# Kernel tuning notes

Hardware: AMD Instinct MI355X
Metric: run time of the kernel (lower is better)

The kernel has to match this reference:

```python
import jax, jax.numpy as jnp
import numpy as np
from jax import lax

H_HID, W_HID = 8, 12
N_PAIR = H_HID * W_HID   # 96
NF = 32                  # mlp_nfilters
C_FEAT = 512 + 2         # phi_im channels + (x,y) coords


def _conv_relu(x, w, b):
    # 3x3 conv, stride 1, SAME padding (SingleConvBlock), then ReLU
    y = lax.conv_general_dilated(x, w, (1, 1), 'SAME',
                                 dimension_numbers=('NCHW', 'OIHW', 'NCHW'))
    return jax.nn.relu(y + b[None, :, None, None])


def _maxpool2(x):
    return lax.reduce_window(x, -jnp.inf, lax.max, (1, 1, 2, 2), (1, 1, 2, 2), 'VALID')


def setup_inputs() -> dict:
    key = jax.random.key(0)
    ks = jax.random.split(key, 16)
    d = {}
    d['x'] = jax.random.normal(ks[0], (4, 3, 64, 96), jnp.float32)
    d['sen_embed'] = jax.random.normal(ks[1], (4, 384), jnp.float32)

    def p(k, shape, fan_in):
        return (jax.random.normal(k, shape, jnp.float32) / np.float32(np.sqrt(fan_in)))

    d['enc1_w'] = p(ks[2], (64, 3, 3, 3), 3 * 9);      d['enc1_b'] = p(ks[3], (64,), 64)
    d['enc2_w'] = p(ks[4], (128, 64, 3, 3), 64 * 9);   d['enc2_b'] = p(ks[5], (128,), 128)
    d['enc3_w'] = p(ks[6], (256, 128, 3, 3), 128 * 9); d['enc3_b'] = p(ks[7], (256,), 256)
    d['enc4_w'] = p(ks[8], (512, 256, 3, 3), 256 * 9); d['enc4_b'] = p(ks[9], (512,), 512)
    d['g1_w'] = p(ks[10], (1412, 256), 1412);          d['g1_b'] = p(ks[11], (256,), 256)
    d['g2_w'] = p(ks[12], (256, 256), 256);            d['g2_b'] = p(ks[13], (256,), 256)
    d['g3_w'] = p(ks[14], (256, N_PAIR * NF), 256);    d['g3_b'] = p(ks[15], (N_PAIR * NF,), N_PAIR * NF)
    return d


def _forward(x, sen_embed, enc1_w, enc1_b, enc2_w, enc2_b, enc3_w, enc3_b,
             enc4_w, enc4_b, g1_w, g1_b, g2_w, g2_b, g3_w, g3_b):
    # ---- conv encoder ----
    e1 = _conv_relu(x, enc1_w, enc1_b)                     # [B,64,64,96]
    e2 = _conv_relu(_maxpool2(e1), enc2_w, enc2_b)         # [B,128,32,48]
    e3 = _conv_relu(_maxpool2(e2), enc3_w, enc3_b)         # [B,256,16,24]
    phi_im = _conv_relu(_maxpool2(e3), enc4_w, enc4_b)     # [B,512,8,12]
    B = phi_im.shape[0]

    # ---- coordinate grid (matches torch.meshgrid default 'ij' then reshape) ----
    xc = jnp.linspace(-1.0, 1.0, W_HID, dtype=phi_im.dtype)
    yc = jnp.linspace(-1.0, 1.0, H_HID, dtype=phi_im.dtype)
    xg, yg = jnp.meshgrid(xc, yc, indexing='ij')           # each [12,8]
    coord = jnp.stack([xg.reshape(H_HID, W_HID), yg.reshape(H_HID, W_HID)], axis=0)
    coord = jnp.broadcast_to(coord[None], (B, 2, H_HID, W_HID))

    # per-location features F: [B, n_pair, 514]
    F = jnp.concatenate([phi_im, coord], axis=1).reshape(B, C_FEAT, N_PAIR).transpose(0, 2, 1)

    # ---- all-pairs relation network ----
    # pair feature at (a,c) = concat(F[c], F[a], sen_embed); exploit linearity of first
    # Linear to avoid materializing the [B,n,n,1412] concat tensor (same math).
    A, Bm, Cm = g1_w[:C_FEAT], g1_w[C_FEAT:2 * C_FEAT], g1_w[2 * C_FEAT:]
    u = F @ A                                # i-part,  [B,n,256]
    v = F @ Bm                               # j-part,  [B,n,256]
    ws = sen_embed @ Cm + g1_b               # sentence part, [B,256]
    h1 = jax.nn.relu(u[:, None, :, :] + v[:, :, None, :] + ws[:, None, None, :])  # [B,n,n,256]
    h2 = jax.nn.relu(h1 @ g2_w + g2_b)                                           # [B,n,n,256]
    out = jax.nn.relu(h2 @ g3_w + g3_b)                                          # [B,n,n,3072]

    # sum over all n_pair^2 pairs, reshape to feature map [B,32,8,12]
    phi = out.sum(axis=(1, 2)).reshape(B, NF, H_HID, W_HID)
    return phi


def reference(x, sen_embed, enc1_w, enc1_b, enc2_w, enc2_b, enc3_w, enc3_b,
              enc4_w, enc4_b, g1_w, g1_b, g2_w, g2_b, g3_w, g3_b):
    return _forward(x, sen_embed, enc1_w, enc1_b, enc2_w, enc2_b, enc3_w, enc3_b,
                    enc4_w, enc4_b, g1_w, g1_b, g2_w, g2_b, g3_w, g3_b)
```

## Files before the change

kernel.cpp:

```cpp
#include <hip/hip_runtime.h>
#include <hip/hip_bf16.h>

using bf16 = __hip_bfloat16;
typedef __attribute__((ext_vector_type(8))) short short8;
typedef __attribute__((ext_vector_type(4))) float f32x4;

static __device__ __forceinline__ bf16 f2b(float x) { return __float2bfloat16(x); }
static __device__ __forceinline__ float b2f(bf16 x) { return __bfloat162float(x); }
static __device__ __forceinline__ short fb(float x) {
  bf16 h = __float2bfloat16(fmaxf(x, 0.f));
  return *(short*)&h;
}

static __device__ __forceinline__ void gload_lds16(const void* g, void* l) {
  auto gp = (const __attribute__((address_space(1))) unsigned int*)g;
  auto lp = (__attribute__((address_space(3))) unsigned int*)l;
  __builtin_amdgcn_global_load_lds(gp, lp, 16, 0, 0);
}

__global__ void prep_all_kernel(const float* __restrict__ x, const float* __restrict__ w1,
                                const float* __restrict__ b1, bf16* __restrict__ p1,
                                const float* __restrict__ w2, const float* __restrict__ w3,
                                const float* __restrict__ w4, const float* __restrict__ g1w,
                                const float* __restrict__ sen, float* __restrict__ outz,
                                bf16* __restrict__ w2r, bf16* __restrict__ w3r,
                                bf16* __restrict__ w4r, bf16* __restrict__ wuv,
                                bf16* __restrict__ Fe, float* __restrict__ zb,
                                const float* __restrict__ g2w, const float* __restrict__ g3w,
                                bf16* __restrict__ w2t, bf16* __restrict__ w3t) {
  __shared__ float wl[27 * 64];
  __shared__ bf16 tt[32][33];
  int bid = blockIdx.x;
  int tid = threadIdx.x;
  if (bid < 1536) {
    const int H = 64, W = 96, HW = H * W;
    for (int idx = tid; idx < 27 * 64; idx += 256) {
      int k = idx >> 6, oc_ = idx & 63;
      wl[idx] = w1[oc_ * 27 + k];
    }
    __syncthreads();
    int oc = tid & 63;
    int pp = bid * 4 + (tid >> 6);
    int b = pp / 1536, rem = pp - b * 1536;
    int yp = rem / 48, xp = rem - yp * 48;
    int y0 = 2 * yp - 1, x0 = 2 * xp - 1;
    float win[3][4][4];
    #pragma unroll
    for (int ic = 0; ic < 3; ++ic) {
      const float* xsrc = x + ((size_t)b * 3 + ic) * HW;
      #pragma unroll
      for (int dy = 0; dy < 4; ++dy) {
        int yy = y0 + dy;
        #pragma unroll
        for (int dx = 0; dx < 4; ++dx) {
          int xx = x0 + dx;
          win[ic][dy][dx] = (yy >= 0 && yy < H && xx >= 0 && xx < W) ? xsrc[yy * W + xx] : 0.f;
        }
      }
    }
    float cmax = -1e30f;
    #pragma unroll
    for (int sy = 0; sy < 2; ++sy)
      #pragma unroll
      for (int sx = 0; sx < 2; ++sx) {
        float acc = 0.f;
        #pragma unroll
        for (int ic = 0; ic < 3; ++ic)
          #pragma unroll
          for (int ky = 0; ky < 3; ++ky)
            #pragma unroll
            for (int kx = 0; kx < 3; ++kx)
              acc += win[ic][sy + ky][sx + kx] * wl[(ic * 9 + ky * 3 + kx) * 64 + oc];
        cmax = fmaxf(cmax, acc);
      }
    p1[(size_t)pp * 64 + oc] = f2b(fmaxf(cmax + b1[oc], 0.f));
  } else if (bid < 9601) {
    const int S1 = 73728, S2 = S1 + 294912, S3 = S2 + 1179648, S4 = S3 + 442368,
              S5 = S4 + 12288, S6 = S5 + 24576, S7 = S6 + 36864, S8 = S7 + 64;
    int i = (bid - 1536) * 256 + tid;
    if (i < S1) {
      int j = i, K = 576, IC = 64;
      int oc = j / K, r = j - oc * K, tap = r / IC, ic = r - tap * IC;
      w2r[j] = f2b(w2[((size_t)oc * IC + ic) * 9 + tap]);
    } else if (i < S2) {
      int j = i - S1, K = 1152, IC = 128;
      int oc = j / K, r = j - oc * K, tap = r / IC, ic = r - tap * IC;
      w3r[j] = f2b(w3[((size_t)oc * IC + ic) * 9 + tap]);
    } else if (i < S3) {
      int j = i - S2, K = 2304, IC = 256;
      int oc = j / K, r = j - oc * K, tap = r / IC, ic = r - tap * IC;
      w4r[j] = f2b(w4[((size_t)oc * IC + ic) * 9 + tap]);
    } else if (i < S4) {
      int j = i - S3;
      int n = j / 576, c = j - n * 576;
      float val = 0.f;
      if (n < 256)      { if (c < 514) val = g1w[(size_t)c * 256 + n]; }
      else if (n < 512) { if (c < 514) val = g1w[(size_t)(514 + c) * 256 + (n - 256)]; }
      else              { if (c < 384) val = g1w[(size_t)(1028 + c) * 256 + (n - 512)]; }
      wuv[j] = f2b(val);
    } else if (i < S5) {
      outz[i - S4] = 0.f;
    } else if (i < S6) {
      int j = i - S5;
      int r = j >> 6, cc = j & 63;
      int p = r % 96;
      float val = 0.f;
      if (cc == 0) val = -1.0f + 2.0f * (float)(p / 8) / 11.0f;
      else if (cc == 1) val = -1.0f + 2.0f * (float)(p % 8) / 7.0f;
      Fe[(size_t)r * 576 + 512 + cc] = f2b(val);
    } else if (i < S7) {
      int j = i - S6;
      int r = j / 576, c = j - r * 576;
      float val = (r < 4 && c < 384) ? sen[r * 384 + c] : 0.f;
      Fe[(size_t)(384 + r) * 576 + c] = f2b(val);
    } else if (i < S8) {
      zb[i - S7] = 0.f;
    }
  } else {
    int b2 = bid - 9601;
    const float* in;
    bf16* out;
    int R = 256, C, c0, r0;
    if (b2 < 64) { in = g2w; out = w2t; C = 256; c0 = (b2 & 7) * 32; r0 = (b2 >> 3) * 32; }
    else { b2 -= 64; in = g3w; out = w3t; C = 3072; c0 = (b2 % 96) * 32; r0 = (b2 / 96) * 32; }
    int xq = tid & 31, yq = tid >> 5;
    for (int yy = yq; yy < 32; yy += 8) {
      int r = r0 + yy, c = c0 + xq;
      if (r < R && c < C) tt[yy][xq] = f2b(in[(size_t)r * C + c]);
    }
    __syncthreads();
    for (int yy = yq; yy < 32; yy += 8) {
      int c = c0 + yy, r = r0 + xq;
      if (r < R && c < C) out[(size_t)c * R + r] = tt[xq][yy];
    }
  }
}

template <int CBITS, bool POOL>
__launch_bounds__(256)
__global__ void gemm_conv_kernel(const bf16* __restrict__ pin, const bf16* __restrict__ Wt,
                                 const float* __restrict__ bias, bf16* __restrict__ outb,
                                 const bf16* __restrict__ zbuf,
                                 int Hi, int Wi, int N, int ldout) {
  const int C = 1 << CBITS;
  const int K = 9 << CBITS;
  int m0 = blockIdx.y * 64, n0 = blockIdx.x * 64;
  __shared__ __align__(16) short A_lds[2][64 * 64];
  __shared__ __align__(16) short B_lds[2][64 * 64];
  int tid = threadIdx.x, w = tid >> 6, l = tid & 63;
  int quad = l >> 4, l16 = l & 15;
  f32x4 acc[4];
  #pragma unroll
  for (int nt = 0; nt < 4; ++nt)
    #pragma unroll
    for (int e = 0; e < 4; ++e) acc[nt][e] = 0.f;

  int lrow = l >> 3;
  int c_sw = (l & 7) ^ lrow;
  int ybase[2], xbase[2], bidx[2];
  #pragma unroll
  for (int i = 0; i < 2; ++i) {
    int row = m0 + w * 16 + i * 8 + lrow;
    if (POOL) {
      int pg = row >> 2, sub = row & 3;
      int Wh = Wi >> 1, HW2 = (Hi >> 1) * Wh;
      int b = pg / HW2, rem = pg - b * HW2;
      int py = rem / Wh, px = rem - py * Wh;
      bidx[i] = b; ybase[i] = 2 * py + (sub >> 1); xbase[i] = 2 * px + (sub & 1);
    } else {
      int HW = Hi * Wi;
      int b = row / HW, pix = row - b * HW;
      int yy = pix / Wi;
      bidx[i] = b; ybase[i] = yy; xbase[i] = pix - yy * Wi;
    }
  }
  const bf16* bg = Wt + (size_t)(n0 + w * 16 + lrow) * K + c_sw * 8;

  auto stage = [&](int kc, int buf) {
    int colt = kc + c_sw * 8;
    int tap = colt >> CBITS, cc = colt & (C - 1);
    int ty = tap / 3, tx = tap - 3 * ty;
    short* al = &A_lds[buf][((size_t)w * 128 + l) * 8];
    short* bl = &B_lds[buf][((size_t)w * 128 + l) * 8];
    #pragma unroll
    for (int i = 0; i < 2; ++i) {
      int yy = ybase[i] + ty - 1, xx = xbase[i] + tx - 1;
      const bf16* asrc = (yy >= 0 && yy < Hi && xx >= 0 && xx < Wi)
          ? pin + ((((size_t)(bidx[i] * Hi + yy)) * Wi + xx) << CBITS) + cc
          : zbuf;
      gload_lds16(asrc, al + i * 512);
      gload_lds16(bg + kc + (size_t)i * 8 * K, bl + i * 512);
    }
  };

  stage(0, 0);
  const int NK = K >> 6;
  for (int ik = 0; ik < NK; ++ik) {
    int buf = ik & 1;
    __syncthreads();
    if (ik + 1 < NK) stage((ik + 1) * 64, buf ^ 1);
    #pragma unroll
    for (int ks = 0; ks < 64; ks += 32) {
      int cb = (ks >> 3) + quad;
      int mr = w * 16 + l16;
      short8 af = *(const short8*)&A_lds[buf][mr * 64 + ((cb ^ (mr & 7)) * 8)];
      #pragma unroll
      for (int nt = 0; nt < 4; ++nt) {
        int nr = nt * 16 + l16;
        short8 bf2 = *(const short8*)&B_lds[buf][nr * 64 + ((cb ^ (nr & 7)) * 8)];
        acc[nt] = __builtin_amdgcn_mfma_f32_16x16x32_bf16(af, bf2, acc[nt], 0, 0, 0);
      }
    }
  }
  if (POOL) {
    int pg = (m0 + w * 16 + quad * 4) >> 2;
    #pragma unroll
    for (int nt = 0; nt < 4; ++nt) {
      int gcol = n0 + nt * 16 + l16;
      float bv = bias[gcol];
      float m = fmaxf(fmaxf(acc[nt][0], acc[nt][1]), fmaxf(acc[nt][2], acc[nt][3]));
      outb[(size_t)pg * N + gcol] = f2b(fmaxf(m + bv, 0.f));
    }
  } else {
    #pragma unroll
    for (int nt = 0; nt < 4; ++nt) {
      int gcol = n0 + nt * 16 + l16;
      float bv = bias[gcol];
      #pragma unroll
      for (int r = 0; r < 4; ++r) {
        int grow = m0 + w * 16 + quad * 4 + r;
        outb[(size_t)grow * ldout + gcol] = f2b(fmaxf(acc[nt][r] + bv, 0.f));
      }
    }
  }
}

__launch_bounds__(256)
__global__ void gemm64_kernel(const bf16* __restrict__ A, const bf16* __restrict__ Wt,
                              float* __restrict__ outf, int K, int ldout) {
  int m0 = blockIdx.y * 64, n0 = blockIdx.x * 64;
  __shared__ __align__(16) short A_lds[2][64 * 64];
  __shared__ __align__(16) short B_lds[2][64 * 64];
  int tid = threadIdx.x, w = tid >> 6, l = tid & 63;
  int quad = l >> 4, l16 = l & 15;
  f32x4 acc[4];
  #pragma unroll
  for (int nt = 0; nt < 4; ++nt)
    #pragma unroll
    for (int e = 0; e < 4; ++e) acc[nt][e] = 0.f;

  int lrow = l >> 3;
  int c_sw = (l & 7) ^ lrow;
  const bf16* ag = A + (size_t)(m0 + w * 16 + lrow) * K + c_sw * 8;
  const bf16* bg = Wt + (size_t)(n0 + w * 16 + lrow) * K + c_sw * 8;

  auto stage = [&](int kc, int buf) {
    short* al = &A_lds[buf][((size_t)w * 128 + l) * 8];
    short* bl = &B_lds[buf][((size_t)w * 128 + l) * 8];
    #pragma unroll
    for (int i = 0; i < 2; ++i) {
      gload_lds16(ag + kc + (size_t)i * 8 * K, al + i * 512);
      gload_lds16(bg + kc + (size_t)i * 8 * K, bl + i * 512);
    }
  };

  stage(0, 0);
  const int NK = K >> 6;
  for (int ik = 0; ik < NK; ++ik) {
    int buf = ik & 1;
    __syncthreads();
    if (ik + 1 < NK) stage((ik + 1) * 64, buf ^ 1);
    #pragma unroll
    for (int ks = 0; ks < 64; ks += 32) {
      int cb = (ks >> 3) + quad;
      int mr = w * 16 + l16;
      short8 af = *(const short8*)&A_lds[buf][mr * 64 + ((cb ^ (mr & 7)) * 8)];
      #pragma unroll
      for (int nt = 0; nt < 4; ++nt) {
        int nr = nt * 16 + l16;
        short8 bf2 = *(const short8*)&B_lds[buf][nr * 64 + ((cb ^ (nr & 7)) * 8)];
        acc[nt] = __builtin_amdgcn_mfma_f32_16x16x32_bf16(af, bf2, acc[nt], 0, 0, 0);
      }
    }
  }
  #pragma unroll
  for (int nt = 0; nt < 4; ++nt) {
    int gcol = n0 + nt * 16 + l16;
    #pragma unroll
    for (int r = 0; r < 4; ++r) {
      int grow = m0 + w * 16 + quad * 4 + r;
      outf[(size_t)grow * ldout + gcol] = acc[nt][r];
    }
  }
}

__launch_bounds__(256)
__global__ void gemm2_kernel(const float* __restrict__ uvws, const float* __restrict__ g1b,
                             const bf16* __restrict__ w2t, const float* __restrict__ g2b,
                             bf16* __restrict__ h2) {
  int b = blockIdx.z;
  int m0 = blockIdx.y * 128;
  int n0 = blockIdx.x * 128;
  __shared__ __align__(16) short A_lds[128 * 64];
  __shared__ __align__(16) short B_lds[128 * 64];
  __shared__ __align__(16) float wsl[256];
  int tid = threadIdx.x, w = tid >> 6, l = tid & 63;
  int quad = l >> 4, l16 = l & 15;
  int mw = (w >> 1) * 64, nw = (w & 1) * 64;
  f32x4 acc[4][4];
  #pragma unroll
  for (int i = 0; i < 4; ++i)
    #pragma unroll
    for (int j = 0; j < 4; ++j)
      #pragma unroll
      for (int e = 0; e < 4; ++e) acc[i][j][e] = 0.f;

  wsl[tid] = uvws[(size_t)(384 + b) * 768 + 512 + tid] + g1b[tid];

  int lrow = l >> 3;
  int c_sw = (l & 7) ^ lrow;
  const bf16* bg = w2t + (size_t)(n0 + w * 32 + lrow) * 256 + c_sw * 8;
  short* bl = B_lds + ((size_t)w * 256 + l) * 8;

  int row = tid >> 1, ks0 = (tid & 1) * 32;
  int m = m0 + row;
  int i_idx = m / 96, j_idx = m - i_idx * 96;
  const float* up = uvws + (size_t)(b * 96 + j_idx) * 768 + ks0;
  const float* vp = uvws + (size_t)(b * 96 + i_idx) * 768 + 256 + ks0;
  __syncthreads();

  for (int kc = 0; kc < 256; kc += 64) {
    if (kc) __syncthreads();
    #pragma unroll
    for (int i = 0; i < 4; ++i)
      gload_lds16(bg + kc + (size_t)i * 8 * 256, bl + i * 512);
    {
      const float4* u4 = (const float4*)(up + kc);
      const float4* v4 = (const float4*)(vp + kc);
      const float4* w4 = (const float4*)&wsl[kc + ks0];
      #pragma unroll
      for (int ch = 0; ch < 4; ++ch) {
        short8 pack;
        #pragma unroll
        for (int q = 0; q < 2; ++q) {
          float4 uu = u4[ch * 2 + q], vv = v4[ch * 2 + q], ww = w4[ch * 2 + q];
          pack[q * 4 + 0] = fb(uu.x + vv.x + ww.x);
          pack[q * 4 + 1] = fb(uu.y + vv.y + ww.y);
          pack[q * 4 + 2] = fb(uu.z + vv.z + ww.z);
          pack[q * 4 + 3] = fb(uu.w + vv.w + ww.w);
        }
        int lc = (ks0 >> 3) + ch;
        *(short8*)&A_lds[row * 64 + ((lc ^ (row & 7)) * 8)] = pack;
      }
    }
    __syncthreads();
    #pragma unroll
    for (int ks = 0; ks < 64; ks += 32) {
      int cb = (ks >> 3) + quad;
      short8 af[4], bfr[4];
      #pragma unroll
      for (int mt = 0; mt < 4; ++mt) {
        int mr = mw + mt * 16 + l16;
        af[mt] = *(const short8*)&A_lds[mr * 64 + ((cb ^ (mr & 7)) * 8)];
      }
      #pragma unroll
      for (int nt = 0; nt < 4; ++nt) {
        int nr = nw + nt * 16 + l16;
        bfr[nt] = *(const short8*)&B_lds[nr * 64 + ((cb ^ (nr & 7)) * 8)];
      }
      #pragma unroll
      for (int mt = 0; mt < 4; ++mt)
        #pragma unroll
        for (int nt = 0; nt < 4; ++nt)
          acc[mt][nt] = __builtin_amdgcn_mfma_f32_16x16x32_bf16(af[mt], bfr[nt], acc[mt][nt], 0, 0, 0);
    }
  }
  bf16* h2b = h2 + (size_t)b * 9216 * 256;
  #pragma unroll
  for (int nt = 0; nt < 4; ++nt) {
    int gcol = n0 + nw + nt * 16 + l16;
    float bias = g2b[gcol];
    #pragma unroll
    for (int mt = 0; mt < 4; ++mt) {
      #pragma unroll
      for (int r = 0; r < 4; ++r) {
        int grow = m0 + mw + mt * 16 + quad * 4 + r;
        h2b[(size_t)grow * 256 + gcol] = f2b(fmaxf(acc[mt][nt][r] + bias, 0.f));
      }
    }
  }
}

__launch_bounds__(256)
__global__ void gemm3_kernel(const bf16* __restrict__ h2, const bf16* __restrict__ w3t,
                             const float* __restrict__ g3b, float* __restrict__ phi) {
  int g = blockIdx.x;
  int x = g & 7, s = g >> 3;
  int grp = s / 24;
  int nIdx = s - grp * 24;
  int mb = grp * 8 + x;
  int b = mb / 72;
  int m0 = (mb - b * 72) * 128;
  int n0 = nIdx * 128;
  __shared__ __align__(16) short A_lds[128 * 64];
  __shared__ __align__(16) short B_lds[128 * 64];
  int tid = threadIdx.x, w = tid >> 6, l = tid & 63;
  int quad = l >> 4, l16 = l & 15;
  int mw = (w >> 1) * 64, nw = (w & 1) * 64;
  f32x4 acc[4][4];
  #pragma unroll
  for (int i = 0; i < 4; ++i)
    #pragma unroll
    for (int j = 0; j < 4; ++j)
      #pragma unroll
      for (int e = 0; e < 4; ++e) acc[i][j][e] = 0.f;

  const int K = 256;
  int lrow = l >> 3;
  int c_sw = (l & 7) ^ lrow;
  const bf16* ag = h2 + (size_t)(b * 9216 + m0 + w * 32 + lrow) * K + c_sw * 8;
  const bf16* bg = w3t + (size_t)(n0 + w * 32 + lrow) * K + c_sw * 8;
  short* al = A_lds + ((size_t)w * 256 + l) * 8;
  short* bl = B_lds + ((size_t)w * 256 + l) * 8;

  for (int kc = 0; kc < K; kc += 64) {
    if (kc) __syncthreads();
    #pragma unroll
    for (int i = 0; i < 4; ++i) {
      gload_lds16(ag + kc + (size_t)i * 8 * K, al + i * 512);
      gload_lds16(bg + kc + (size_t)i * 8 * K, bl + i * 512);
    }
    __syncthreads();
    #pragma unroll
    for (int ks = 0; ks < 64; ks += 32) {
      int cb = (ks >> 3) + quad;
      short8 af[4], bfr[4];
      #pragma unroll
      for (int mt = 0; mt < 4; ++mt) {
        int mr = mw + mt * 16 + l16;
        af[mt] = *(const short8*)&A_lds[mr * 64 + ((cb ^ (mr & 7)) * 8)];
      }
      #pragma unroll
      for (int nt = 0; nt < 4; ++nt) {
        int nr = nw + nt * 16 + l16;
        bfr[nt] = *(const short8*)&B_lds[nr * 64 + ((cb ^ (nr & 7)) * 8)];
      }
      #pragma unroll
      for (int mt = 0; mt < 4; ++mt)
        #pragma unroll
        for (int nt = 0; nt < 4; ++nt)
          acc[mt][nt] = __builtin_amdgcn_mfma_f32_16x16x32_bf16(af[mt], bfr[nt], acc[mt][nt], 0, 0, 0);
    }
  }
  #pragma unroll
  for (int nt = 0; nt < 4; ++nt) {
    int gcol = n0 + nw + nt * 16 + l16;
    float bias = g3b[gcol];
    float s2 = 0.f;
    #pragma unroll
    for (int mt = 0; mt < 4; ++mt)
      #pragma unroll
      for (int r = 0; r < 4; ++r)
        s2 += fmaxf(acc[mt][nt][r] + bias, 0.f);
    s2 += __shfl_xor(s2, 16, 64);
    s2 += __shfl_xor(s2, 32, 64);
    if (quad == 0) atomicAdd(&phi[b * 3072 + gcol], s2);
  }
}

extern "C" void kernel_launch(void* const* d_in, const int* in_sizes, int n_in,
                              void* d_out, int out_size, void* d_ws, size_t ws_size,
                              hipStream_t stream) {
  const float* x   = (const float*)d_in[0];
  const float* sen = (const float*)d_in[1];
  const float* w1  = (const float*)d_in[2];
  const float* b1  = (const float*)d_in[3];
  const float* w2  = (const float*)d_in[4];
  const float* b2  = (const float*)d_in[5];
  const float* w3  = (const float*)d_in[6];
  const float* b3  = (const float*)d_in[7];
  const float* w4  = (const float*)d_in[8];
  const float* b4  = (const float*)d_in[9];
  const float* g1w = (const float*)d_in[10];
  const float* g1b = (const float*)d_in[11];
  const float* g2w = (const float*)d_in[12];
  const float* g2b = (const float*)d_in[13];
  const float* g3w = (const float*)d_in[14];
  const float* g3b = (const float*)d_in[15];
  float* out = (float*)d_out;

  char* wsp = (char*)d_ws;
  size_t off = 0;
  auto alloc = [&](size_t bytes) {
    char* p = wsp + off;
    off += (bytes + 255) & ~(size_t)255;
    return (void*)p;
  };
  bf16* p1   = (bf16*)alloc((size_t)6144 * 64 * 2);
  bf16* p2   = (bf16*)alloc((size_t)1536 * 128 * 2);
  bf16* p3   = (bf16*)alloc((size_t)384 * 256 * 2);
  bf16* Fe   = (bf16*)alloc((size_t)448 * 576 * 2);
  bf16* wuv  = (bf16*)alloc((size_t)768 * 576 * 2);
  float* uvws = (float*)alloc((size_t)448 * 768 * 4);
  bf16* w2r  = (bf16*)alloc((size_t)128 * 576 * 2);
  bf16* w3r  = (bf16*)alloc((size_t)256 * 1152 * 2);
  bf16* w4r  = (bf16*)alloc((size_t)512 * 2304 * 2);
  bf16* w2t  = (bf16*)alloc((size_t)256 * 256 * 2);
  bf16* w3t  = (bf16*)alloc((size_t)3072 * 256 * 2);
  bf16* h2   = (bf16*)alloc((size_t)4 * 9216 * 256 * 2);
  float* zbuf = (float*)alloc((size_t)256);

  prep_all_kernel<<<dim3(10433), 256, 0, stream>>>(x, w1, b1, p1, w2, w3, w4, g1w, sen, out,
                                                   w2r, w3r, w4r, wuv, Fe, zbuf, g2w, g3w, w2t, w3t);

  gemm_conv_kernel<6, true><<<dim3(2, 96), 256, 0, stream>>>(p1, w2r, b2, p2, (const bf16*)zbuf, 32, 48, 128, 128);
  gemm_conv_kernel<7, true><<<dim3(4, 24), 256, 0, stream>>>(p2, w3r, b3, p3, (const bf16*)zbuf, 16, 24, 256, 256);
  gemm_conv_kernel<8, false><<<dim3(8, 6), 256, 0, stream>>>(p3, w4r, b4, Fe, (const bf16*)zbuf, 8, 12, 512, 576);

  gemm64_kernel<<<dim3(12, 7), 256, 0, stream>>>(Fe, wuv, uvws, 576, 768);
  gemm2_kernel<<<dim3(2, 72, 4), 256, 0, stream>>>(uvws, g1b, w2t, g2b, h2);
  gemm3_kernel<<<dim3(6912), 256, 0, stream>>>(h2, w3t, g3b, out);
}
```

Baseline: 240.7 us.

## Fuse all stages into one persistent cooperative kernel with grid syncs

Replaces the seven separate kernel launches (prep, three conv GEMMs, uv GEMM, pair GEMM2, GEMM3) with a single cooperative persistent kernel. Blocks loop over per-stage task indices and use grid.sync between stages, sharing one LDS allocation. This removes inter-launch gaps and launch overhead. The cost is grid-wide barriers, a single combined register/LDS footprint that may lower occupancy for the heavier stages, and fixed persistent grid sizing (up to 3 blocks per CU).

```diff
diff --git a/kernel.cpp b/kernel.cpp
--- a/kernel.cpp
+++ b/kernel.cpp
@@ -1,12 +1,13 @@
 #include <hip/hip_runtime.h>
 #include <hip/hip_bf16.h>
-
+#include <hip/hip_cooperative_groups.h>
+
+namespace cg = cooperative_groups;
 using bf16 = __hip_bfloat16;
 typedef __attribute__((ext_vector_type(8))) short short8;
 typedef __attribute__((ext_vector_type(4))) float f32x4;
 
 static __device__ __forceinline__ bf16 f2b(float x) { return __float2bfloat16(x); }
-static __device__ __forceinline__ float b2f(bf16 x) { return __bfloat162float(x); }
 static __device__ __forceinline__ short fb(float x) {
   bf16 h = __float2bfloat16(fmaxf(x, 0.f));
   return *(short*)&h;
@@ -18,36 +19,33 @@
   __builtin_amdgcn_global_load_lds(gp, lp, 16, 0, 0);
 }
 
-__global__ void prep_all_kernel(const float* __restrict__ x, const float* __restrict__ w1,
-                                const float* __restrict__ b1, bf16* __restrict__ p1,
-                                const float* __restrict__ w2, const float* __restrict__ w3,
-                                const float* __restrict__ w4, const float* __restrict__ g1w,
-                                const float* __restrict__ sen, float* __restrict__ outz,
-                                bf16* __restrict__ w2r, bf16* __restrict__ w3r,
-                                bf16* __restrict__ w4r, bf16* __restrict__ wuv,
-                                bf16* __restrict__ Fe, float* __restrict__ zb,
-                                const float* __restrict__ g2w, const float* __restrict__ g3w,
-                                bf16* __restrict__ w2t, bf16* __restrict__ w3t) {
-  __shared__ float wl[27 * 64];
-  __shared__ bf16 tt[32][33];
-  int bid = blockIdx.x;
-  int tid = threadIdx.x;
-  if (bid < 1536) {
+struct MegaParams {
+  const float *x, *sen, *w1, *b1, *w2, *b2, *w3, *b3, *w4, *b4;
+  const float *g1w, *g1b, *g2w, *g2b, *g3w, *g3b;
+  float* out;
+  bf16 *p1, *p2, *p3, *Fe, *wuv, *w2r, *w3r, *w4r, *w2t, *w3t, *h2;
+  float *uvws, *zbuf;
+};
+
+static __device__ void prep_task(const MegaParams& P, int t, int tid, short* LA, short* LB) {
+  if (t < 1536) {
+    float* wl = (float*)LA;
+    __syncthreads();
     const int H = 64, W = 96, HW = H * W;
     for (int idx = tid; idx < 27 * 64; idx += 256) {
       int k = idx >> 6, oc_ = idx & 63;
-      wl[idx] = w1[oc_ * 27 + k];
+      wl[idx] = P.w1[oc_ * 27 + k];
     }
     __syncthreads();
     int oc = tid & 63;
-    int pp = bid * 4 + (tid >> 6);
+    int pp = t * 4 + (tid >> 6);
     int b = pp / 1536, rem = pp - b * 1536;
     int yp = rem / 48, xp = rem - yp * 48;
     int y0 = 2 * yp - 1, x0 = 2 * xp - 1;
     float win[3][4][4];
     #pragma unroll
     for (int ic = 0; ic < 3; ++ic) {
-      const float* xsrc = x + ((size_t)b * 3 + ic) * HW;
+      const float* xsrc = P.x + ((size_t)b * 3 + ic) * HW;
       #pragma unroll
       for (int dy = 0; dy < 4; ++dy) {
         int yy = y0 + dy;
@@ -73,33 +71,33 @@
               acc += win[ic][sy + ky][sx + kx] * wl[(ic * 9 + ky * 3 + kx) * 64 + oc];
         cmax = fmaxf(cmax, acc);
       }
-    p1[(size_t)pp * 64 + oc] = f2b(fmaxf(cmax + b1[oc], 0.f));
-  } else if (bid < 9601) {
+    P.p1[(size_t)pp * 64 + oc] = f2b(fmaxf(cmax + P.b1[oc], 0.f));
+  } else if (t < 9601) {
     const int S1 = 73728, S2 = S1 + 294912, S3 = S2 + 1179648, S4 = S3 + 442368,
               S5 = S4 + 12288, S6 = S5 + 24576, S7 = S6 + 36864, S8 = S7 + 64;
-    int i = (bid - 1536) * 256 + tid;
+    int i = (t - 1536) * 256 + tid;
     if (i < S1) {
       int j = i, K = 576, IC = 64;
       int oc = j / K, r = j - oc * K, tap = r / IC, ic = r - tap * IC;
-      w2r[j] = f2b(w2[((size_t)oc * IC + ic) * 9 + tap]);
+      P.w2r[j] = f2b(P.w2[((size_t)oc * IC + ic) * 9 + tap]);
     } else if (i < S2) {
       int j = i - S1, K = 1152, IC = 128;
       int oc = j / K, r = j - oc * K, tap = r / IC, ic = r - tap * IC;
-      w3r[j] = f2b(w3[((size_t)oc * IC + ic) * 9 + tap]);
+      P.w3r[j] = f2b(P.w3[((size_t)oc * IC + ic) * 9 + tap]);
     } else if (i < S3) {
       int j = i - S2, K = 2304, IC = 256;
       int oc = j / K, r = j - oc * K, tap = r / IC, ic = r - tap * IC;
-      w4r[j] = f2b(w4[((size_t)oc * IC + ic) * 9 + tap]);
+      P.w4r[j] = f2b(P.w4[((size_t)oc * IC + ic) * 9 + tap]);
     } else if (i < S4) {
       int j = i - S3;
       int n = j / 576, c = j - n * 576;
       float val = 0.f;
-      if (n < 256)      { if (c < 514) val = g1w[(size_t)c * 256 + n]; }
-      else if (n < 512) { if (c < 514) val = g1w[(size_t)(514 + c) * 256 + (n - 256)]; }
-      else              { if (c < 384) val = g1w[(size_t)(1028 + c) * 256 + (n - 512)]; }
-      wuv[j] = f2b(val);
+      if (n < 256)      { if (c < 514) val = P.g1w[(size_t)c * 256 + n]; }
+      else if (n < 512) { if (c < 514) val = P.g1w[(size_t)(514 + c) * 256 + (n - 256)]; }
+      else              { if (c < 384) val = P.g1w[(size_t)(1028 + c) * 256 + (n - 512)]; }
+      P.wuv[j] = f2b(val);
     } else if (i < S5) {
-      outz[i - S4] = 0.f;
+      P.out[i - S4] = 0.f;
     } else if (i < S6) {
       int j = i - S5;
       int r = j >> 6, cc = j & 63;
@@ -107,22 +105,24 @@
       float val = 0.f;
       if (cc == 0) val = -1.0f + 2.0f * (float)(p / 8) / 11.0f;
       else if (cc == 1) val = -1.0f + 2.0f * (float)(p % 8) / 7.0f;
-      Fe[(size_t)r * 576 + 512 + cc] = f2b(val);
+      P.Fe[(size_t)r * 576 + 512 + cc] = f2b(val);
     } else if (i < S7) {
       int j = i - S6;
       int r = j / 576, c = j - r * 576;
-      float val = (r < 4 && c < 384) ? sen[r * 384 + c] : 0.f;
-      Fe[(size_t)(384 + r) * 576 + c] = f2b(val);
+      float val = (r < 4 && c < 384) ? P.sen[r * 384 + c] : 0.f;
+      P.Fe[(size_t)(384 + r) * 576 + c] = f2b(val);
     } else if (i < S8) {
-      zb[i - S7] = 0.f;
+      P.zbuf[i - S7] = 0.f;
     }
   } else {
-    int b2 = bid - 9601;
+    bf16 (*tt)[33] = (bf16(*)[33])LB;
+    __syncthreads();
+    int b2 = t - 9601;
     const float* in;
     bf16* out;
     int R = 256, C, c0, r0;
-    if (b2 < 64) { in = g2w; out = w2t; C = 256; c0 = (b2 & 7) * 32; r0 = (b2 >> 3) * 32; }
-    else { b2 -= 64; in = g3w; out = w3t; C = 3072; c0 = (b2 % 96) * 32; r0 = (b2 / 96) * 32; }
+    if (b2 < 64) { in = P.g2w; out = P.w2t; C = 256; c0 = (b2 & 7) * 32; r0 = (b2 >> 3) * 32; }
+    else { b2 -= 64; in = P.g3w; out = P.w3t; C = 3072; c0 = (b2 % 96) * 32; r0 = (b2 / 96) * 32; }
     int xq = tid & 31, yq = tid >> 5;
     for (int yy = yq; yy < 32; yy += 8) {
       int r = r0 + yy, c = c0 + xq;
@@ -137,17 +137,13 @@
 }
 
 template <int CBITS, bool POOL>
-__launch_bounds__(256)
-__global__ void gemm_conv_kernel(const bf16* __restrict__ pin, const bf16* __restrict__ Wt,
-                                 const float* __restrict__ bias, bf16* __restrict__ outb,
-                                 const bf16* __restrict__ zbuf,
-                                 int Hi, int Wi, int N, int ldout) {
+static __device__ void conv_task(const bf16* pin, const bf16* Wt, const float* bias,
+                                 bf16* outb, const bf16* zbuf, int Hi, int Wi, int N, int ldout,
+                                 int nIdx, int mIdx, int tid, short* LA, short* LB) {
   const int C = 1 << CBITS;
   const int K = 9 << CBITS;
-  int m0 = blockIdx.y * 64, n0 = blockIdx.x * 64;
-  __shared__ __align__(16) short A_lds[2][64 * 64];
-  __shared__ __align__(16) short B_lds[2][64 * 64];
-  int tid = threadIdx.x, w = tid >> 6, l = tid & 63;
+  int m0 = mIdx * 64, n0 = nIdx * 64;
+  int w = tid >> 6, l = tid & 63;
   int quad = l >> 4, l16 = l & 15;
   f32x4 acc[4];
   #pragma unroll
@@ -180,8 +176,8 @@
     int colt = kc + c_sw * 8;
     int tap = colt >> CBITS, cc = colt & (C - 1);
     int ty = tap / 3, tx = tap - 3 * ty;
-    short* al = &A_lds[buf][((size_t)w * 128 + l) * 8];
-    short* bl = &B_lds[buf][((size_t)w * 128 + l) * 8];
+    short* al = LA + buf * 4096 + ((size_t)w * 128 + l) * 8;
+    short* bl = LB + buf * 4096 + ((size_t)w * 128 + l) * 8;
     #pragma unroll
     for (int i = 0; i < 2; ++i) {
       int yy = ybase[i] + ty - 1, xx = xbase[i] + tx - 1;
@@ -193,6 +189,7 @@
     }
   };
 
+  __syncthreads();
   stage(0, 0);
   const int NK = K >> 6;
   for (int ik = 0; ik < NK; ++ik) {
@@ -203,11 +200,11 @@
     for (int ks = 0; ks < 64; ks += 32) {
       int cb = (ks >> 3) + quad;
       int mr = w * 16 + l16;
-      short8 af = *(const short8*)&A_lds[buf][mr * 64 + ((cb ^ (mr & 7)) * 8)];
+      short8 af = *(const short8*)&LA[buf * 4096 + mr * 64 + ((cb ^ (mr & 7)) * 8)];
       #pragma unroll
       for (int nt = 0; nt < 4; ++nt) {
         int nr = nt * 16 + l16;
-        short8 bf2 = *(const short8*)&B_lds[buf][nr * 64 + ((cb ^ (nr & 7)) * 8)];
+        short8 bf2 = *(const short8*)&LB[buf * 4096 + nr * 64 + ((cb ^ (nr & 7)) * 8)];
         acc[nt] = __builtin_amdgcn_mfma_f32_16x16x32_bf16(af, bf2, acc[nt], 0, 0, 0);
       }
     }
@@ -235,13 +232,10 @@
   }
 }
 
-__launch_bounds__(256)
-__global__ void gemm64_kernel(const bf16* __restrict__ A, const bf16* __restrict__ Wt,
-                              float* __restrict__ outf, int K, int ldout) {
-  int m0 = blockIdx.y * 64, n0 = blockIdx.x * 64;
-  __shared__ __align__(16) short A_lds[2][64 * 64];
-  __shared__ __align__(16) short B_lds[2][64 * 64];
-  int tid = threadIdx.x, w = tid >> 6, l = tid & 63;
+static __device__ void gemm64_task(const bf16* A, const bf16* Wt, float* outf, int K, int ldout,
+                                   int nIdx, int mIdx, int tid, short* LA, short* LB) {
+  int m0 = mIdx * 64, n0 = nIdx * 64;
+  int w = tid >> 6, l = tid & 63;
   int quad = l >> 4, l16 = l & 15;
   f32x4 acc[4];
   #pragma unroll
@@ -255,8 +249,8 @@
   const bf16* bg = Wt + (size_t)(n0 + w * 16 + lrow) * K + c_sw * 8;
 
   auto stage = [&](int kc, int buf) {
-    short* al = &A_lds[buf][((size_t)w * 128 + l) * 8];
-    short* bl = &B_lds[buf][((size_t)w * 128 + l) * 8];
+    short* al = LA + buf * 4096 + ((size_t)w * 128 + l) * 8;
+    short* bl = LB + buf * 4096 + ((size_t)w * 128 + l) * 8;
     #pragma unroll
     for (int i = 0; i < 2; ++i) {
       gload_lds16(ag + kc + (size_t)i * 8 * K, al + i * 512);
@@ -264,6 +258,7 @@
     }
   };
 
+  __syncthreads();
   stage(0, 0);
   const int NK = K >> 6;
   for (int ik = 0; ik < NK; ++ik) {
@@ -274,11 +269,11 @@
     for (int ks = 0; ks < 64; ks += 32) {
       int cb = (ks >> 3) + quad;
       int mr = w * 16 + l16;
-      short8 af = *(const short8*)&A_lds[buf][mr * 64 + ((cb ^ (mr & 7)) * 8)];
+      short8 af = *(const short8*)&LA[buf * 4096 + mr * 64 + ((cb ^ (mr & 7)) * 8)];
       #pragma unroll
       for (int nt = 0; nt < 4; ++nt) {
         int nr = nt * 16 + l16;
-        short8 bf2 = *(const short8*)&B_lds[buf][nr * 64 + ((cb ^ (nr & 7)) * 8)];
+        short8 bf2 = *(const short8*)&LB[buf * 4096 + nr * 64 + ((cb ^ (nr & 7)) * 8)];
         acc[nt] = __builtin_amdgcn_mfma_f32_16x16x32_bf16(af, bf2, acc[nt], 0, 0, 0);
       }
     }
@@ -294,17 +289,15 @@
   }
 }
 
-__launch_bounds__(256)
-__global__ void gemm2_kernel(const float* __restrict__ uvws, const float* __restrict__ g1b,
-                             const bf16* __restrict__ w2t, const float* __restrict__ g2b,
-                             bf16* __restrict__ h2) {
-  int b = blockIdx.z;
-  int m0 = blockIdx.y * 128;
-  int n0 = blockIdx.x * 128;
-  __shared__ __align__(16) short A_lds[128 * 64];
-  __shared__ __align__(16) short B_lds[128 * 64];
-  __shared__ __align__(16) float wsl[256];
-  int tid = threadIdx.x, w = tid >> 6, l = tid & 63;
+static __device__ void gemm2_task(const MegaParams& P, int t, int tid,
+                                  short* LA, short* LB, float* wsl) {
+  int nIdx = t & 1;
+  int rest = t >> 1;
+  int mIdx = rest % 72;
+  int b = rest / 72;
+  int m0 = mIdx * 128;
+  int n0 = nIdx * 128;
+  int w = tid >> 6, l = tid & 63;
   int quad = l >> 4, l16 = l & 15;
   int mw = (w >> 1) * 64, nw = (w & 1) * 64;
   f32x4 acc[4][4];
@@ -315,18 +308,19 @@
       #pragma unroll
       for (int e = 0; e < 4; ++e) acc[i][j][e] = 0.f;
 
-  wsl[tid] = uvws[(size_t)(384 + b) * 768 + 512 + tid] + g1b[tid];
+  __syncthreads();
+  wsl[tid] = P.uvws[(size_t)(384 + b) * 768 + 512 + tid] + P.g1b[tid];
 
   int lrow = l >> 3;
   int c_sw = (l & 7) ^ lrow;
-  const bf16* bg = w2t + (size_t)(n0 + w * 32 + lrow) * 256 + c_sw * 8;
-  short* bl = B_lds + ((size_t)w * 256 + l) * 8;
+  const bf16* bg = P.w2t + (size_t)(n0 + w * 32 + lrow) * 256 + c_sw * 8;
+  short* bl = LB + ((size_t)w * 256 + l) * 8;
 
   int row = tid >> 1, ks0 = (tid & 1) * 32;
   int m = m0 + row;
   int i_idx = m / 96, j_idx = m - i_idx * 96;
-  const float* up = uvws + (size_t)(b * 96 + j_idx) * 768 + ks0;
-  const float* vp = uvws + (size_t)(b * 96 + i_idx) * 768 + 256 + ks0;
+  const float* up = P.uvws + (size_t)(b * 96 + j_idx) * 768 + ks0;
+  const float* vp = P.uvws + (size_t)(b * 96 + i_idx) * 768 + 256 + ks0;
   __syncthreads();
 
   for (int kc = 0; kc < 256; kc += 64) {
@@ -350,7 +344,7 @@
           pack[q * 4 + 3] = fb(uu.w + vv.w + ww.w);
         }
         int lc = (ks0 >> 3) + ch;
-        *(short8*)&A_lds[row * 64 + ((lc ^ (row & 7)) * 8)] = pack;
+        *(short8*)&LA[row * 64 + ((lc ^ (row & 7)) * 8)] = pack;
       }
     }
     __syncthreads();
@@ -361,12 +355,12 @@
       #pragma unroll
       for (int mt = 0; mt < 4; ++mt) {
         int mr = mw + mt * 16 + l16;
-        af[mt] = *(const short8*)&A_lds[mr * 64 + ((cb ^ (mr & 7)) * 8)];
+        af[mt] = *(const short8*)&LA[mr * 64 + ((cb ^ (mr & 7)) * 8)];
       }
       #pragma unroll
       for (int nt = 0; nt < 4; ++nt) {
         int nr = nw + nt * 16 + l16;
-        bfr[nt] = *(const short8*)&B_lds[nr * 64 + ((cb ^ (nr & 7)) * 8)];
+        bfr[nt] = *(const short8*)&LB[nr * 64 + ((cb ^ (nr & 7)) * 8)];
       }
       #pragma unroll
       for (int mt = 0; mt < 4; ++mt)
@@ -375,11 +369,11 @@
           acc[mt][nt] = __builtin_amdgcn_mfma_f32_16x16x32_bf16(af[mt], bfr[nt], acc[mt][nt], 0, 0, 0);
     }
   }
-  bf16* h2b = h2 + (size_t)b * 9216 * 256;
+  bf16* h2b = P.h2 + (size_t)b * 9216 * 256;
   #pragma unroll
   for (int nt = 0; nt < 4; ++nt) {
     int gcol = n0 + nw + nt * 16 + l16;
-    float bias = g2b[gcol];
+    float bias = P.g2b[gcol];
     #pragma unroll
     for (int mt = 0; mt < 4; ++mt) {
       #pragma unroll
@@ -391,10 +385,7 @@
   }
 }
 
-__launch_bounds__(256)
-__global__ void gemm3_kernel(const bf16* __restrict__ h2, const bf16* __restrict__ w3t,
-                             const float* __restrict__ g3b, float* __restrict__ phi) {
-  int g = blockIdx.x;
+static __device__ void gemm3_task(const MegaParams& P, int g, int tid, short* LA, short* LB) {
   int x = g & 7, s = g >> 3;
   int grp = s / 24;
   int nIdx = s - grp * 24;
@@ -402,9 +393,7 @@
   int b = mb / 72;
   int m0 = (mb - b * 72) * 128;
   int n0 = nIdx * 128;
-  __shared__ __align__(16) short A_lds[128 * 64];
-  __shared__ __align__(16) short B_lds[128 * 64];
-  int tid = threadIdx.x, w = tid >> 6, l = tid & 63;
+  int w = tid >> 6, l = tid & 63;
   int quad = l >> 4, l16 = l & 15;
   int mw = (w >> 1) * 64, nw = (w & 1) * 64;
   f32x4 acc[4][4];
@@ -418,11 +407,12 @@
   const int K = 256;
   int lrow = l >> 3;
   int c_sw = (l & 7) ^ lrow;
-  const bf16* ag = h2 + (size_t)(b * 9216 + m0 + w * 32 + lrow) * K + c_sw * 8;
-  const bf16* bg = w3t + (size_t)(n0 + w * 32 + lrow) * K + c_sw * 8;
-  short* al = A_lds + ((size_t)w * 256 + l) * 8;
-  short* bl = B_lds + ((size_t)w * 256 + l) * 8;
-
+  const bf16* ag = P.h2 + (size_t)(b * 9216 + m0 + w * 32 + lrow) * K + c_sw * 8;
+  const bf16* bg = P.w3t + (size_t)(n0 + w * 32 + lrow) * K + c_sw * 8;
+  short* al = LA + ((size_t)w * 256 + l) * 8;
+  short* bl = LB + ((size_t)w * 256 + l) * 8;
+
+  __syncthreads();
   for (int kc = 0; kc < K; kc += 64) {
     if (kc) __syncthreads();
     #pragma unroll
@@ -438,12 +428,12 @@
       #pragma unroll
       for (int mt = 0; mt < 4; ++mt) {
         int mr = mw + mt * 16 + l16;
-        af[mt] = *(const short8*)&A_lds[mr * 64 + ((cb ^ (mr & 7)) * 8)];
+        af[mt] = *(const short8*)&LA[mr * 64 + ((cb ^ (mr & 7)) * 8)];
       }
       #pragma unroll
       for (int nt = 0; nt < 4; ++nt) {
         int nr = nw + nt * 16 + l16;
-        bfr[nt] = *(const short8*)&B_lds[nr * 64 + ((cb ^ (nr & 7)) * 8)];
+        bfr[nt] = *(const short8*)&LB[nr * 64 + ((cb ^ (nr & 7)) * 8)];
       }
       #pragma unroll
       for (int mt = 0; mt < 4; ++mt)
@@ -455,7 +445,7 @@
   #pragma unroll
   for (int nt = 0; nt < 4; ++nt) {
     int gcol = n0 + nw + nt * 16 + l16;
-    float bias = g3b[gcol];
+    float bias = P.g3b[gcol];
     float s2 = 0.f;
     #pragma unroll
     for (int mt = 0; mt < 4; ++mt)
@@ -464,31 +454,42 @@
         s2 += fmaxf(acc[mt][nt][r] + bias, 0.f);
     s2 += __shfl_xor(s2, 16, 64);
     s2 += __shfl_xor(s2, 32, 64);
-    if (quad == 0) atomicAdd(&phi[b * 3072 + gcol], s2);
-  }
+    if (quad == 0) atomicAdd(&P.out[b * 3072 + gcol], s2);
+  }
+}
+
+__global__ void __launch_bounds__(256) mega_kernel(MegaParams P) {
+  __shared__ __align__(16) short LA[8192];
+  __shared__ __align__(16) short LB[8192];
+  __shared__ float wsl[256];
+  cg::grid_group grid = cg::this_grid();
+  int bid = blockIdx.x, nb = gridDim.x, tid = threadIdx.x;
+
+  for (int t = bid; t < 10433; t += nb) prep_task(P, t, tid, LA, LB);
+  grid.sync();
+  for (int t = bid; t < 192; t += nb)
+    conv_task<6, true>(P.p1, P.w2r, P.b2, P.p2, (const bf16*)P.zbuf, 32, 48, 128, 128,
+                       t & 1, t >> 1, tid, LA, LB);
+  grid.sync();
+  for (int t = bid; t < 96; t += nb)
+    conv_task<7, true>(P.p2, P.w3r, P.b3, P.p3, (const bf16*)P.zbuf, 16, 24, 256, 256,
+                       t & 3, t >> 2, tid, LA, LB);
+  grid.sync();
+  for (int t = bid; t < 48; t += nb)
+    conv_task<8, false>(P.p3, P.w4r, P.b4, P.Fe, (const bf16*)P.zbuf, 8, 12, 512, 576,
+                        t & 7, t >> 3, tid, LA, LB);
+  grid.sync();
+  for (int t = bid; t < 84; t += nb)
+    gemm64_task(P.Fe, P.wuv, P.uvws, 576, 768, t % 12, t / 12, tid, LA, LB);
+  grid.sync();
+  for (int t = bid; t < 576; t += nb) gemm2_task(P, t, tid, LA, LB, wsl);
+  grid.sync();
+  for (int t = bid; t < 6912; t += nb) gemm3_task(P, t, tid, LA, LB);
 }
 
 extern "C" void kernel_launch(void* const* d_in, const int* in_sizes, int n_in,
                               void* d_out, int out_size, void* d_ws, size_t ws_size,
                               hipStream_t stream) {
-  const float* x   = (const float*)d_in[0];
-  const float* sen = (const float*)d_in[1];
-  const float* w1  = (const float*)d_in[2];
-  const float* b1  = (const float*)d_in[3];
-  const float* w2  = (const float*)d_in[4];
-  const float* b2  = (const float*)d_in[5];
-  const float* w3  = (const float*)d_in[6];
-  const float* b3  = (const float*)d_in[7];
-  const float* w4  = (const float*)d_in[8];
-  const float* b4  = (const float*)d_in[9];
-  const float* g1w = (const float*)d_in[10];
-  const float* g1b = (const float*)d_in[11];
-  const float* g2w = (const float*)d_in[12];
-  const float* g2b = (const float*)d_in[13];
-  const float* g3w = (const float*)d_in[14];
-  const float* g3b = (const float*)d_in[15];
-  float* out = (float*)d_out;
-
   char* wsp = (char*)d_ws;
   size_t off = 0;
   auto alloc = [&](size_t bytes) {
@@ -496,28 +497,44 @@
     off += (bytes + 255) & ~(size_t)255;
     return (void*)p;
   };
-  bf16* p1   = (bf16*)alloc((size_t)6144 * 64 * 2);
-  bf16* p2   = (bf16*)alloc((size_t)1536 * 128 * 2);
-  bf16* p3   = (bf16*)alloc((size_t)384 * 256 * 2);
-  bf16* Fe   = (bf16*)alloc((size_t)448 * 576 * 2);
-  bf16* wuv  = (bf16*)alloc((size_t)768 * 576 * 2);
-  float* uvws = (float*)alloc((size_t)448 * 768 * 4);
-  bf16* w2r  = (bf16*)alloc((size_t)128 * 576 * 2);
-  bf16* w3r  = (bf16*)alloc((size_t)256 * 1152 * 2);
-  bf16* w4r  = (bf16*)alloc((size_t)512 * 2304 * 2);
-  bf16* w2t  = (bf16*)alloc((size_t)256 * 256 * 2);
-  bf16* w3t  = (bf16*)alloc((size_t)3072 * 256 * 2);
-  bf16* h2   = (bf16*)alloc((size_t)4 * 9216 * 256 * 2);
-  float* zbuf = (float*)alloc((size_t)256);
-
-  prep_all_kernel<<<dim3(10433), 256, 0, stream>>>(x, w1, b1, p1, w2, w3, w4, g1w, sen, out,
-                                                   w2r, w3r, w4r, wuv, Fe, zbuf, g2w, g3w, w2t, w3t);
-
-  gemm_conv_kernel<6, true><<<dim3(2, 96), 256, 0, stream>>>(p1, w2r, b2, p2, (const bf16*)zbuf, 32, 48, 128, 128);
-  gemm_conv_kernel<7, true><<<dim3(4, 24), 256, 0, stream>>>(p2, w3r, b3, p3, (const bf16*)zbuf, 16, 24, 256, 256);
-  gemm_conv_kernel<8, false><<<dim3(8, 6), 256, 0, stream>>>(p3, w4r, b4, Fe, (const bf16*)zbuf, 8, 12, 512, 576);
-
-  gemm64_kernel<<<dim3(12, 7), 256, 0, stream>>>(Fe, wuv, uvws, 576, 768);
-  gemm2_kernel<<<dim3(2, 72, 4), 256, 0, stream>>>(uvws, g1b, w2t, g2b, h2);
-  gemm3_kernel<<<dim3(6912), 256, 0, stream>>>(h2, w3t, g3b, out);
-}
+  MegaParams P;
+  P.x   = (const float*)d_in[0];
+  P.sen = (const float*)d_in[1];
+  P.w1  = (const float*)d_in[2];
+  P.b1  = (const float*)d_in[3];
+  P.w2  = (const float*)d_in[4];
+  P.b2  = (const float*)d_in[5];
+  P.w3  = (const float*)d_in[6];
+  P.b3  = (const float*)d_in[7];
+  P.w4  = (const float*)d_in[8];
+  P.b4  = (const float*)d_in[9];
+  P.g1w = (const float*)d_in[10];
+  P.g1b = (const float*)d_in[11];
+  P.g2w = (const float*)d_in[12];
+  P.g2b = (const float*)d_in[13];
+  P.g3w = (const float*)d_in[14];
+  P.g3b = (const float*)d_in[15];
+  P.out = (float*)d_out;
+  P.p1   = (bf16*)alloc((size_t)6144 * 64 * 2);
+  P.p2   = (bf16*)alloc((size_t)1536 * 128 * 2);
+  P.p3   = (bf16*)alloc((size_t)384 * 256 * 2);
+  P.Fe   = (bf16*)alloc((size_t)448 * 576 * 2);
+  P.wuv  = (bf16*)alloc((size_t)768 * 576 * 2);
+  P.uvws = (float*)alloc((size_t)448 * 768 * 4);
+  P.w2r  = (bf16*)alloc((size_t)128 * 576 * 2);
+  P.w3r  = (bf16*)alloc((size_t)256 * 1152 * 2);
+  P.w4r  = (bf16*)alloc((size_t)512 * 2304 * 2);
+  P.w2t  = (bf16*)alloc((size_t)256 * 256 * 2);
+  P.w3t  = (bf16*)alloc((size_t)3072 * 256 * 2);
+  P.h2   = (bf16*)alloc((size_t)4 * 9216 * 256 * 2);
+  P.zbuf = (float*)alloc((size_t)256);
+
+  int maxB = 0;
+  (void)hipOccupancyMaxActiveBlocksPerMultiprocessor(&maxB, mega_kernel, 256, 0);
+  if (maxB < 1) maxB = 1;
+  if (maxB > 3) maxB = 3;
+  int nb = maxB * 256;
+
+  void* kargs[] = { (void*)&P };
+  (void)hipLaunchCooperativeKernel((void*)mega_kernel, dim3(nb), dim3(256), kargs, 0, stream);
+}
```

New measurement: 515.5 us. +114.2%, slower.

## Run first conv layer as padded MFMA implicit GEMM instead of scalar FMA

Applied to the files above, without the earlier changes.

Moves the first 3x3 conv with fused maxpool out of the prep kernel's scalar per-thread loops. The input is repacked to NHWC bf16 with channels padded to 8 and the weights to 16 taps times 8 channels. It then runs on the existing MFMA implicit-GEMM conv kernel, with a TAPS template parameter that masks the padded taps. This replaces fp32 scalar FMAs with matrix instructions, at the cost of an extra kernel launch, the padding waste and bf16 rounding of the input and weights.

```diff
diff --git a/kernel.cpp b/kernel.cpp
--- a/kernel.cpp
+++ b/kernel.cpp
@@ -19,7 +19,7 @@
 }
 
 __global__ void prep_all_kernel(const float* __restrict__ x, const float* __restrict__ w1,
-                                const float* __restrict__ b1, bf16* __restrict__ p1,
+                                bf16* __restrict__ x8, bf16* __restrict__ w1r,
                                 const float* __restrict__ w2, const float* __restrict__ w3,
                                 const float* __restrict__ w4, const float* __restrict__ g1w,
                                 const float* __restrict__ sen, float* __restrict__ outz,
@@ -28,58 +28,26 @@
                                 bf16* __restrict__ Fe, float* __restrict__ zb,
                                 const float* __restrict__ g2w, const float* __restrict__ g3w,
                                 bf16* __restrict__ w2t, bf16* __restrict__ w3t) {
-  __shared__ float wl[27 * 64];
   __shared__ bf16 tt[32][33];
   int bid = blockIdx.x;
   int tid = threadIdx.x;
-  if (bid < 1536) {
-    const int H = 64, W = 96, HW = H * W;
-    for (int idx = tid; idx < 27 * 64; idx += 256) {
-      int k = idx >> 6, oc_ = idx & 63;
-      wl[idx] = w1[oc_ * 27 + k];
-    }
-    __syncthreads();
-    int oc = tid & 63;
-    int pp = bid * 4 + (tid >> 6);
-    int b = pp / 1536, rem = pp - b * 1536;
-    int yp = rem / 48, xp = rem - yp * 48;
-    int y0 = 2 * yp - 1, x0 = 2 * xp - 1;
-    float win[3][4][4];
-    #pragma unroll
-    for (int ic = 0; ic < 3; ++ic) {
-      const float* xsrc = x + ((size_t)b * 3 + ic) * HW;
-      #pragma unroll
-      for (int dy = 0; dy < 4; ++dy) {
-        int yy = y0 + dy;
-        #pragma unroll
-        for (int dx = 0; dx < 4; ++dx) {
-          int xx = x0 + dx;
-          win[ic][dy][dx] = (yy >= 0 && yy < H && xx >= 0 && xx < W) ? xsrc[yy * W + xx] : 0.f;
-        }
-      }
-    }
-    float cmax = -1e30f;
-    #pragma unroll
-    for (int sy = 0; sy < 2; ++sy)
-      #pragma unroll
-      for (int sx = 0; sx < 2; ++sx) {
-        float acc = 0.f;
-        #pragma unroll
-        for (int ic = 0; ic < 3; ++ic)
-          #pragma unroll
-          for (int ky = 0; ky < 3; ++ky)
-            #pragma unroll
-            for (int kx = 0; kx < 3; ++kx)
-              acc += win[ic][sy + ky][sx + kx] * wl[(ic * 9 + ky * 3 + kx) * 64 + oc];
-        cmax = fmaxf(cmax, acc);
-      }
-    p1[(size_t)pp * 64 + oc] = f2b(fmaxf(cmax + b1[oc], 0.f));
-  } else if (bid < 9601) {
-    const int S1 = 73728, S2 = S1 + 294912, S3 = S2 + 1179648, S4 = S3 + 442368,
-              S5 = S4 + 12288, S6 = S5 + 24576, S7 = S6 + 36864, S8 = S7 + 64;
-    int i = (bid - 1536) * 256 + tid;
-    if (i < S1) {
-      int j = i, K = 576, IC = 64;
+  if (bid < 768) {
+    int i = bid * 256 + tid;
+    int c = i & 7, pix = i >> 3;
+    int b = pix / 6144, rem = pix - b * 6144;
+    float val = (c < 3) ? x[(size_t)(b * 3 + c) * 6144 + rem] : 0.f;
+    x8[i] = f2b(val);
+  } else if (bid < 8865) {
+    const int SW1 = 8192, S1 = SW1 + 73728, S2 = S1 + 294912, S3 = S2 + 1179648,
+              S4 = S3 + 442368, S5 = S4 + 12288, S6 = S5 + 24576, S7 = S6 + 36864,
+              S8 = S7 + 64;
+    int i = (bid - 768) * 256 + tid;
+    if (i < SW1) {
+      int oc = i >> 7, r = i & 127, tap = r >> 3, c = r & 7;
+      float val = (tap < 9 && c < 3) ? w1[(size_t)(oc * 3 + c) * 9 + tap] : 0.f;
+      w1r[i] = f2b(val);
+    } else if (i < S1) {
+      int j = i - SW1, K = 576, IC = 64;
       int oc = j / K, r = j - oc * K, tap = r / IC, ic = r - tap * IC;
       w2r[j] = f2b(w2[((size_t)oc * IC + ic) * 9 + tap]);
     } else if (i < S2) {
@@ -117,7 +85,7 @@
       zb[i - S7] = 0.f;
     }
   } else {
-    int b2 = bid - 9601;
+    int b2 = bid - 8865;
     const float* in;
     bf16* out;
     int R = 256, C, c0, r0;
@@ -136,14 +104,14 @@
   }
 }
 
-template <int CBITS, bool POOL>
+template <int CBITS, bool POOL, int TAPS = 9>
 __launch_bounds__(256)
 __global__ void gemm_conv_kernel(const bf16* __restrict__ pin, const bf16* __restrict__ Wt,
                                  const float* __restrict__ bias, bf16* __restrict__ outb,
                                  const bf16* __restrict__ zbuf,
                                  int Hi, int Wi, int N, int ldout) {
   const int C = 1 << CBITS;
-  const int K = 9 << CBITS;
+  const int K = TAPS << CBITS;
   int m0 = blockIdx.y * 64, n0 = blockIdx.x * 64;
   __shared__ __align__(16) short A_lds[2][64 * 64];
   __shared__ __align__(16) short B_lds[2][64 * 64];
@@ -185,7 +153,8 @@
     #pragma unroll
     for (int i = 0; i < 2; ++i) {
       int yy = ybase[i] + ty - 1, xx = xbase[i] + tx - 1;
-      const bf16* asrc = (yy >= 0 && yy < Hi && xx >= 0 && xx < Wi)
+      bool ok = (tap < 9) && (yy >= 0) && (yy < Hi) && (xx >= 0) && (xx < Wi);
+      const bf16* asrc = ok
           ? pin + ((((size_t)(bidx[i] * Hi + yy)) * Wi + xx) << CBITS) + cc
           : zbuf;
       gload_lds16(asrc, al + i * 512);
@@ -496,6 +465,8 @@
     off += (bytes + 255) & ~(size_t)255;
     return (void*)p;
   };
+  bf16* x8   = (bf16*)alloc((size_t)24576 * 8 * 2);
+  bf16* w1r  = (bf16*)alloc((size_t)64 * 128 * 2);
   bf16* p1   = (bf16*)alloc((size_t)6144 * 64 * 2);
   bf16* p2   = (bf16*)alloc((size_t)1536 * 128 * 2);
   bf16* p3   = (bf16*)alloc((size_t)384 * 256 * 2);
@@ -510,9 +481,10 @@
   bf16* h2   = (bf16*)alloc((size_t)4 * 9216 * 256 * 2);
   float* zbuf = (float*)alloc((size_t)256);
 
-  prep_all_kernel<<<dim3(10433), 256, 0, stream>>>(x, w1, b1, p1, w2, w3, w4, g1w, sen, out,
-                                                   w2r, w3r, w4r, wuv, Fe, zbuf, g2w, g3w, w2t, w3t);
-
+  prep_all_kernel<<<dim3(9697), 256, 0, stream>>>(x, w1, x8, w1r, w2, w3, w4, g1w, sen, out,
+                                                  w2r, w3r, w4r, wuv, Fe, zbuf, g2w, g3w, w2t, w3t);
+
+  gemm_conv_kernel<3, true, 16><<<dim3(1, 384), 256, 0, stream>>>(x8, w1r, b1, p1, (const bf16*)zbuf, 64, 96, 64, 64);
   gemm_conv_kernel<6, true><<<dim3(2, 96), 256, 0, stream>>>(p1, w2r, b2, p2, (const bf16*)zbuf, 32, 48, 128, 128);
   gemm_conv_kernel<7, true><<<dim3(4, 24), 256, 0, stream>>>(p2, w3r, b3, p3, (const bf16*)zbuf, 16, 24, 256, 256);
   gemm_conv_kernel<8, false><<<dim3(8, 6), 256, 0, stream>>>(p3, w4r, b4, Fe, (const bf16*)zbuf, 8, 12, 512, 576);
```

Result: no change. 242.2 us (+0.6%).
